# Performance work log

Measured on AMD Instinct MI355X. Metric: run time of the kernel, lower is better.

## Reference

```python
import jax, jax.numpy as jnp
import numpy as np

DIM = 1024
N_HEADS = 16
HEAD_DIM = DIM // N_HEADS  # 64
FF_DIM = 4096
BATCH = 2
SEQ = 2048
EPS = 1e-8
ROPE_BASE = 10000.0


def _rope_cos_sin(seq_len, head_dim):
    # inv_freq: [head_dim//2]
    inv_freq = 1.0 / (ROPE_BASE ** (jnp.arange(0, head_dim, 2, dtype=jnp.float32) / head_dim))
    t = jnp.arange(seq_len, dtype=jnp.float32)
    freqs = jnp.einsum('i,j->ij', t, inv_freq)          # [S, D/2]
    emb = jnp.concatenate([freqs, freqs], axis=-1)       # [S, D]
    return jnp.cos(emb), jnp.sin(emb)


def _apply_rope(x, cos, sin):
    # x: [B, S, H, D]; cos/sin: [S, D] -> broadcast [1, S, 1, D]
    d2 = x.shape[-1] // 2
    x1, x2 = x[..., :d2], x[..., d2:]
    cos = cos[None, :, None, :]
    sin = sin[None, :, None, :]
    cos1, cos2 = cos[..., :d2], cos[..., d2:]
    sin1, sin2 = sin[..., :d2], sin[..., d2:]
    return jnp.concatenate([x1 * cos1 - x2 * sin1, x1 * sin2 + x2 * cos2], axis=-1)


def _rmsnorm(x, scale):
    # norm = ||x||_2 * d^{-1/2}; out = scale * x / (norm + eps)
    norm = jnp.sqrt(jnp.sum(x * x, axis=-1, keepdims=True)) * (x.shape[-1] ** -0.5)
    return scale * x / (norm + EPS)


def setup_inputs() -> dict:
    key = jax.random.key(0)
    ks = jax.random.split(key, 10)
    s = lambda fan_in: 1.0 / np.sqrt(fan_in)
    return {
        'x': jax.random.normal(ks[0], (BATCH, SEQ, DIM), dtype=jnp.float32),
        'w_qkv': jax.random.normal(ks[1], (DIM, 3 * DIM), dtype=jnp.float32) * s(DIM),
        'w_attn_out': jax.random.normal(ks[2], (DIM, DIM), dtype=jnp.float32) * s(DIM),
        'w_gate': jax.random.normal(ks[3], (DIM, FF_DIM), dtype=jnp.float32) * s(DIM),
        'b_gate': jax.random.normal(ks[4], (FF_DIM,), dtype=jnp.float32) * 0.01,
        'w_lin': jax.random.normal(ks[5], (DIM, FF_DIM), dtype=jnp.float32) * s(DIM),
        'b_lin': jax.random.normal(ks[6], (FF_DIM,), dtype=jnp.float32) * 0.01,
        'w_ff_out': jax.random.normal(ks[7], (FF_DIM, DIM), dtype=jnp.float32) * s(FF_DIM),
        'scale1': jnp.ones((DIM,), dtype=jnp.float32),
        'scale2': jnp.ones((DIM,), dtype=jnp.float32),
    }


def reference(x, w_qkv, w_attn_out, w_gate, b_gate, w_lin, b_lin, w_ff_out, scale1, scale2):
    B, S, _ = x.shape
    residual = x
    qkv = (x @ w_qkv).reshape(B, S, 3, N_HEADS, HEAD_DIM)
    q, k, v = qkv[:, :, 0], qkv[:, :, 1], qkv[:, :, 2]  # [B, S, H, D]
    cos, sin = _rope_cos_sin(S, HEAD_DIM)
    q = _apply_rope(q, cos, sin)
    k = _apply_rope(k, cos, sin)
    # attention scores [B, H, S, S]
    attn = jnp.einsum('bqhd,bkhd->bhqk', q, k) / np.sqrt(HEAD_DIM).astype(np.float32)
    attn = jax.nn.softmax(attn, axis=-1)
    out = jnp.einsum('bhqk,bkhd->bqhd', attn, v).reshape(B, S, DIM)
    out = out @ w_attn_out
    x = _rmsnorm(residual + out, scale1)
    residual = x
    ff = jax.nn.sigmoid(x @ w_gate + b_gate) * (x @ w_lin + b_lin)
    ff = ff @ w_ff_out
    x = _rmsnorm(residual + ff, scale2)
    return x
```

## Files before the change

### kernel.cpp

```cpp
#include <hip/hip_runtime.h>
#include <stdint.h>

#define DIMN 1024
#define NH 16
#define HD 64
#define FFN 4096
#define BBATCH 2
#define SSEQ 2048
#define MROWS (BBATCH*SSEQ)

typedef __bf16 bf16;
typedef __bf16 bf16x8 __attribute__((ext_vector_type(8)));
typedef __bf16 bf16x4 __attribute__((ext_vector_type(4)));
typedef float f32x4 __attribute__((ext_vector_type(4)));
typedef float f32x16 __attribute__((ext_vector_type(16)));
typedef uint32_t u32x4 __attribute__((ext_vector_type(4)));

#define AS1 __attribute__((address_space(1)))
#define AS3 __attribute__((address_space(3)))

__device__ __forceinline__ void gload16(const bf16* g, bf16* l) {
  __builtin_amdgcn_global_load_lds((AS1 const void*)g, (AS3 void*)l, 16, 0, 0);
}

__device__ __forceinline__ uint32_t pkbf(float a, float b) {
  union { bf16 h[2]; uint32_t u; } x;
  x.h[0] = (bf16)a; x.h[1] = (bf16)b;
  return x.u;
}

__global__ void rope_table_kernel(float* __restrict__ tab) {
  int i = blockIdx.x * blockDim.x + threadIdx.x;
  int s = i >> 5, d = i & 31;
  float invf = exp2f(-(float)d * 0.4152410118609203f);
  float fr = (float)s * invf;
  tab[s*64 + d]      = cosf(fr);
  tab[s*64 + 32 + d] = sinf(fr);
}

__global__ void cast_f32_bf16(const float* __restrict__ in, bf16* __restrict__ out, int n4) {
  int i = blockIdx.x * blockDim.x + threadIdx.x;
  if (i < n4) {
    f32x4 v = ((const f32x4*)in)[i];
    bf16x4 o = {(bf16)v.x, (bf16)v.y, (bf16)v.z, (bf16)v.w};
    ((bf16x4*)out)[i] = o;
  }
}

__global__ __launch_bounds__(256) void transpose_cast_f32_bf16(
    const float* __restrict__ in, bf16* __restrict__ out, int R, int C) {
  __shared__ float t[32][33];
  int bx = blockIdx.x, by = blockIdx.y;
  int x = threadIdx.x, y = threadIdx.y;
  #pragma unroll
  for (int j = 0; j < 4; ++j) {
    int r = by*32 + y*4 + j;
    t[y*4+j][x] = in[(size_t)r*C + bx*32 + x];
  }
  __syncthreads();
  #pragma unroll
  for (int j = 0; j < 4; ++j) {
    int c = bx*32 + y*4 + j;
    out[(size_t)c*R + by*32 + x] = (bf16)t[x][y*4+j];
  }
}

template<int NP>
__global__ __launch_bounds__(256) void rmsnorm_sum_kernel(
    const float* __restrict__ parts, const float* __restrict__ resid,
    const float* __restrict__ sc,
    float* __restrict__ outf, bf16* __restrict__ outb) {
  int row = blockIdx.x;
  int tid = threadIdx.x;
  size_t off = (size_t)row * DIMN;
  f32x4 v = ((const f32x4*)(resid + off))[tid];
  #pragma unroll
  for (int p = 0; p < NP; ++p) {
    f32x4 a = ((const f32x4*)(parts + (size_t)p * MROWS * DIMN + off))[tid];
    v.x += a.x; v.y += a.y; v.z += a.z; v.w += a.w;
  }
  float ss = v.x*v.x + v.y*v.y + v.z*v.z + v.w*v.w;
  #pragma unroll
  for (int m = 1; m < 64; m <<= 1) ss += __shfl_xor(ss, m);
  __shared__ float red[4];
  if ((tid & 63) == 0) red[tid >> 6] = ss;
  __syncthreads();
  float tot = red[0] + red[1] + red[2] + red[3];
  float inv = 1.f / (sqrtf(tot) * 0.03125f + 1e-8f);
  f32x4 s4 = ((const f32x4*)sc)[tid];
  f32x4 o = {v.x*s4.x*inv, v.y*s4.y*inv, v.z*s4.z*inv, v.w*s4.w*inv};
  if (outf) ((f32x4*)(outf + off))[tid] = o;
  if (outb) {
    bf16x4 ob = {(bf16)o.x, (bf16)o.y, (bf16)o.z, (bf16)o.w};
    ((bf16x4*)(outb + off))[tid] = ob;
  }
}

template<int EPI>
__global__ void __launch_bounds__(256) gemm_bt(
    const bf16* __restrict__ A, const bf16* __restrict__ B,
    int M, int N, int K,
    void* __restrict__ o0, void* __restrict__ o1, void* __restrict__ o2,
    const void* __restrict__ a0, const void* __restrict__ a1) {
  __shared__ __align__(16) bf16 sh_a[128*32];
  __shared__ __align__(16) bf16 sh_b[128*32];
  const int tid  = threadIdx.x;
  const int lane = tid & 63;
  const int wid  = tid >> 6;

  int gx  = gridDim.x;
  int bid = blockIdx.y * gx + blockIdx.x;
  int nwg = gx * gridDim.y;
  int cpx = nwg >> 3;
  int swz = (bid & 7) * cpx + (bid >> 3);
  int bxi = swz % gx, byi = swz / gx;

  const int m0 = byi * 128, n0 = bxi * 128;
  const int wm = (wid >> 1) * 64, wn = (wid & 1) * 64;

  const int kb = blockIdx.z;
  const int KC = K / (int)gridDim.z;

  f32x4 acc[4][4] = {};

  const bf16* a_base = A + (size_t)m0 * K + (size_t)kb * KC;
  const bf16* b_base = B + (size_t)n0 * K + (size_t)kb * KC;

  for (int k0 = 0; k0 < KC; k0 += 32) {
    __syncthreads();
    #pragma unroll
    for (int i = 0; i < 2; ++i) {
      int idx = i*256 + tid;
      gload16(a_base + (size_t)(idx >> 2)*K + k0 + (idx & 3)*8, &sh_a[idx*8]);
    }
    #pragma unroll
    for (int i = 0; i < 2; ++i) {
      int idx = i*256 + tid;
      gload16(b_base + (size_t)(idx >> 2)*K + k0 + (idx & 3)*8, &sh_b[idx*8]);
    }
    __syncthreads();
    bf16x8 af[4], bfr[4];
    #pragma unroll
    for (int m = 0; m < 4; ++m)
      af[m] = *(const bf16x8*)&sh_a[(wm + m*16 + (lane & 15))*32 + (lane >> 4)*8];
    #pragma unroll
    for (int n = 0; n < 4; ++n)
      bfr[n] = *(const bf16x8*)&sh_b[(wn + n*16 + (lane & 15))*32 + (lane >> 4)*8];
    #pragma unroll
    for (int m = 0; m < 4; ++m)
      #pragma unroll
      for (int n = 0; n < 4; ++n)
        acc[m][n] = __builtin_amdgcn_mfma_f32_16x16x32_bf16(af[m], bfr[n], acc[m][n], 0, 0, 0);
  }

  const int rq = (lane >> 4) * 4;
  const int cl = lane & 15;

  if constexpr (EPI == 0) {
    bf16* q_p = (bf16*)o0; bf16* k_p = (bf16*)o1; bf16* v_p = (bf16*)o2;
    const float* rope = (const float*)a0;
    int sec = (n0 + wn) >> 10;
    int h   = ((n0 + wn) & 1023) >> 6;
    const float qsc = (sec == 0) ? 0.18033688011112042f : 1.0f;
    #pragma unroll
    for (int m = 0; m < 4; ++m) {
      #pragma unroll
      for (int reg = 0; reg < 4; ++reg) {
        int r  = m0 + wm + m*16 + rq + reg;
        int b_ = r >> 11, s_ = r & 2047;
        int tile = s_ >> 5;
        size_t tb = ((size_t)(b_*NH + h) * 64 + tile) * 2048;
        if (sec == 2) {
          int kvl = s_ & 31;
          int ks = kvl >> 4, hiv = (kvl >> 3) & 1, jv = kvl & 7;
          #pragma unroll
          for (int n = 0; n < 4; ++n) {
            int half = n >> 1;
            int qlv  = (n & 1) * 16 + cl;
            v_p[tb + (size_t)(ks*2 + half)*512 + (hiv*32 + qlv)*8 + jv] =
                (bf16)acc[m][n][reg];
          }
        } else {
          int qlt = s_ & 31;
          bf16* dst = (sec == 0 ? q_p : k_p);
          int lo = ((cl >> 3) * 32 + qlt) * 8 + (cl & 7);
          #pragma unroll
          for (int n = 0; n < 2; ++n) {
            int d1 = n*16 + cl;
            float c1 = rope[s_*64 + d1];
            float s1 = rope[s_*64 + 32 + d1];
            float x1 = acc[m][n][reg], x2 = acc[m][n+2][reg];
            dst[tb + (size_t)n*512 + lo]       = (bf16)((x1*c1 - x2*s1) * qsc);
            dst[tb + (size_t)(n+2)*512 + lo]   = (bf16)((x1*s1 + x2*c1) * qsc);
          }
        }
      }
    }
  } else if constexpr (EPI == 1) {
    float* op = (float*)o0;
    const float* rp = (const float*)a0;
    #pragma unroll
    for (int m = 0; m < 4; ++m)
      #pragma unroll
      for (int n = 0; n < 4; ++n)
        #pragma unroll
        for (int reg = 0; reg < 4; ++reg) {
          int r = m0 + wm + m*16 + rq + reg;
          int c = n0 + wn + n*16 + cl;
          op[(size_t)r*N + c] = acc[m][n][reg] + rp[(size_t)r*N + c];
        }
  } else if constexpr (EPI == 2) {
    bf16* op = (bf16*)o0;
    const float* bias = (const float*)a0;
    #pragma unroll
    for (int m = 0; m < 4; ++m)
      #pragma unroll
      for (int n = 0; n < 4; ++n)
        #pragma unroll
        for (int reg = 0; reg < 4; ++reg) {
          int r = m0 + wm + m*16 + rq + reg;
          int c = n0 + wn + n*16 + cl;
          float g = acc[m][n][reg] + bias[c];
          op[(size_t)r*N + c] = (bf16)(1.f / (1.f + __expf(-g)));
        }
  } else if constexpr (EPI == 3) {
    bf16* op = (bf16*)o0;
    const bf16* gp = (const bf16*)a0;
    const float* bias = (const float*)a1;
    #pragma unroll
    for (int m = 0; m < 4; ++m)
      #pragma unroll
      for (int n = 0; n < 4; ++n)
        #pragma unroll
        for (int reg = 0; reg < 4; ++reg) {
          int r = m0 + wm + m*16 + rq + reg;
          int c = n0 + wn + n*16 + cl;
          float l = acc[m][n][reg] + bias[c];
          op[(size_t)r*N + c] = (bf16)((float)gp[(size_t)r*N + c] * l);
        }
  } else if constexpr (EPI == 4) {
    float* op = (float*)o0 + (size_t)kb * M * N;
    #pragma unroll
    for (int m = 0; m < 4; ++m)
      #pragma unroll
      for (int n = 0; n < 4; ++n)
        #pragma unroll
        for (int reg = 0; reg < 4; ++reg) {
          int r = m0 + wm + m*16 + rq + reg;
          int c = n0 + wn + n*16 + cl;
          op[(size_t)r*N + c] = acc[m][n][reg];
        }
  }
}

__global__ void __launch_bounds__(256) attn_kernel(
    const bf16* __restrict__ qf_g, const bf16* __restrict__ kf_g,
    const bf16* __restrict__ vf_g, bf16* __restrict__ ao_g) {
  __shared__ __align__(16) bf16 lds_k[2*2048];
  __shared__ __align__(16) bf16 lds_v[2*2048];
  const int tid  = threadIdx.x;
  const int lane = tid & 63;
  const int qw   = tid >> 6;
  const int hi   = lane >> 5;
  const int ql   = lane & 31;
  const int bh   = blockIdx.y;
  const int b_   = bh >> 4, h = bh & 15;
  const int q0   = blockIdx.x * 128 + qw * 32;
  const int qt   = blockIdx.x * 4 + qw;

  const bf16* qtile = qf_g + ((size_t)bh*64 + qt) * 2048;
  const bf16* kbase = kf_g + (size_t)bh * 64 * 2048;
  const bf16* vbase = vf_g + (size_t)bh * 64 * 2048;

  bf16x8 qf[4];
  #pragma unroll
  for (int ds = 0; ds < 4; ++ds)
    qf[ds] = *(const bf16x8*)&qtile[ds*512 + lane*8];

  f32x16 o0 = {}, o1 = {};
  float lrun = 0.f;

  gload16(kbase + tid*8, &lds_k[tid*8]);
  gload16(vbase + tid*8, &lds_v[tid*8]);

  for (int t = 0; t < 64; ++t) {
    const int cur = (t & 1) * 2048;
    if (t < 63) {
      const int nxt = 2048 - cur;
      gload16(kbase + (size_t)(t+1)*2048 + tid*8, &lds_k[nxt + tid*8]);
      gload16(vbase + (size_t)(t+1)*2048 + tid*8, &lds_v[nxt + tid*8]);
      asm volatile("s_waitcnt vmcnt(2)" ::: "memory");
    } else {
      asm volatile("s_waitcnt vmcnt(0)" ::: "memory");
    }
    __builtin_amdgcn_sched_barrier(0);
    __builtin_amdgcn_s_barrier();
    __builtin_amdgcn_sched_barrier(0);

    f32x16 st = {};
    __builtin_amdgcn_s_setprio(1);
    #pragma unroll
    for (int ds = 0; ds < 4; ++ds) {
      bf16x8 kf = *(const bf16x8*)&lds_k[cur + ds*512 + lane*8];
      st = __builtin_amdgcn_mfma_f32_32x32x16_bf16(kf, qf[ds], st, 0, 0, 0);
    }
    __builtin_amdgcn_s_setprio(0);
    float p[16];
    float psum = 0.f;
    #pragma unroll
    for (int r = 0; r < 16; ++r) { p[r] = __builtin_amdgcn_exp2f(st[r]); psum += p[r]; }
    lrun += psum;

    uint32_t w0 = pkbf(p[0],p[1]),   w1 = pkbf(p[2],p[3]);
    uint32_t w2 = pkbf(p[4],p[5]),   w3 = pkbf(p[6],p[7]);
    uint32_t w4 = pkbf(p[8],p[9]),   w5 = pkbf(p[10],p[11]);
    uint32_t w6 = pkbf(p[12],p[13]), w7 = pkbf(p[14],p[15]);
    asm("v_permlane32_swap_b32 %0, %1" : "+v"(w0), "+v"(w2));
    asm("v_permlane32_swap_b32 %0, %1" : "+v"(w1), "+v"(w3));
    asm("v_permlane32_swap_b32 %0, %1" : "+v"(w4), "+v"(w6));
    asm("v_permlane32_swap_b32 %0, %1" : "+v"(w5), "+v"(w7));

    __builtin_amdgcn_s_setprio(1);
    {
      union { u32x4 u; bf16x8 b; } pu;
      u32x4 pwa = {w0, w1, w2, w3};
      pu.u = pwa;
      bf16x8 v0 = *(const bf16x8*)&lds_v[cur + 0*512 + lane*8];
      bf16x8 v1 = *(const bf16x8*)&lds_v[cur + 1*512 + lane*8];
      o0 = __builtin_amdgcn_mfma_f32_32x32x16_bf16(v0, pu.b, o0, 0, 0, 0);
      o1 = __builtin_amdgcn_mfma_f32_32x32x16_bf16(v1, pu.b, o1, 0, 0, 0);
      u32x4 pwb = {w4, w5, w6, w7};
      pu.u = pwb;
      bf16x8 v2 = *(const bf16x8*)&lds_v[cur + 2*512 + lane*8];
      bf16x8 v3 = *(const bf16x8*)&lds_v[cur + 3*512 + lane*8];
      o0 = __builtin_amdgcn_mfma_f32_32x32x16_bf16(v2, pu.b, o0, 0, 0, 0);
      o1 = __builtin_amdgcn_mfma_f32_32x32x16_bf16(v3, pu.b, o1, 0, 0, 0);
    }
    __builtin_amdgcn_s_setprio(0);

    __builtin_amdgcn_sched_barrier(0);
    __builtin_amdgcn_s_barrier();
    __builtin_amdgcn_sched_barrier(0);
  }

  lrun += __shfl_xor(lrun, 32);
  float inv = 1.f / lrun;
  bf16* aop = ao_g + ((size_t)(b_*SSEQ) + q0 + ql) * DIMN + h*HD;
  #pragma unroll
  for (int g = 0; g < 4; ++g) {
    int dbase = 8*g + 4*hi;
    bf16x4 w0 = {(bf16)(o0[4*g]*inv), (bf16)(o0[4*g+1]*inv),
                 (bf16)(o0[4*g+2]*inv), (bf16)(o0[4*g+3]*inv)};
    *(bf16x4*)&aop[dbase] = w0;
    bf16x4 w1 = {(bf16)(o1[4*g]*inv), (bf16)(o1[4*g+1]*inv),
                 (bf16)(o1[4*g+2]*inv), (bf16)(o1[4*g+3]*inv)};
    *(bf16x4*)&aop[32 + dbase] = w1;
  }
}

extern "C" void kernel_launch(void* const* d_in, const int* in_sizes, int n_in,
                              void* d_out, int out_size, void* d_ws, size_t ws_size,
                              hipStream_t stream) {
  const float* x      = (const float*)d_in[0];
  const float* w_qkv  = (const float*)d_in[1];
  const float* w_ao   = (const float*)d_in[2];
  const float* w_gate = (const float*)d_in[3];
  const float* b_gate = (const float*)d_in[4];
  const float* w_lin  = (const float*)d_in[5];
  const float* b_lin  = (const float*)d_in[6];
  const float* w_ffo  = (const float*)d_in[7];
  const float* scale1 = (const float*)d_in[8];
  const float* scale2 = (const float*)d_in[9];
  float* out = (float*)d_out;
  (void)ws_size; (void)in_sizes; (void)n_in; (void)out_size;

  uint8_t* ws = (uint8_t*)d_ws;
  bf16*  wt_ws   = (bf16*) (ws + 0);
  float* rope_ws = (float*)(ws + 8388608);
  bf16*  xb_ws   = (bf16*) (ws + 8912896);
  bf16*  ao_ws   = (bf16*) (ws + 8912896);
  bf16*  q_ws    = (bf16*) (ws + 17301504);
  bf16*  k_ws    = (bf16*) (ws + 25690112);
  bf16*  v_ws    = (bf16*) (ws + 34078720);
  float* p1_ws   = (float*)(ws + 17301504);
  bf16*  g_ws    = (bf16*) (ws + 50855936);
  bf16*  h1b_ws  = (bf16*) (ws + 84410368);
  bf16*  ffb_ws  = (bf16*) (ws + 8912896);
  float* p2_ws   = (float*)(ws + 42467328);
  float* h1f_ws  = (float*)(ws + 109576192);

  rope_table_kernel<<<256, 256, 0, stream>>>(rope_ws);
  cast_f32_bf16<<<4096, 256, 0, stream>>>(x, xb_ws, MROWS*DIMN/4);
  transpose_cast_f32_bf16<<<dim3(3*DIMN/32, DIMN/32), dim3(32,8), 0, stream>>>(w_qkv, wt_ws, DIMN, 3*DIMN);
  gemm_bt<0><<<dim3(24, 32), 256, 0, stream>>>(xb_ws, wt_ws, MROWS, 3*DIMN, DIMN,
                                               q_ws, k_ws, v_ws, rope_ws, nullptr);
  attn_kernel<<<dim3(16, 32), 256, 0, stream>>>(q_ws, k_ws, v_ws, ao_ws);
  transpose_cast_f32_bf16<<<dim3(DIMN/32, DIMN/32), dim3(32,8), 0, stream>>>(w_ao, wt_ws, DIMN, DIMN);
  gemm_bt<4><<<dim3(8, 32, 2), 256, 0, stream>>>(ao_ws, wt_ws, MROWS, DIMN, DIMN,
                                                 p1_ws, nullptr, nullptr, nullptr, nullptr);
  rmsnorm_sum_kernel<2><<<MROWS, 256, 0, stream>>>(p1_ws, x, scale1, h1f_ws, h1b_ws);
  transpose_cast_f32_bf16<<<dim3(FFN/32, DIMN/32), dim3(32,8), 0, stream>>>(w_gate, wt_ws, DIMN, FFN);
  gemm_bt<2><<<dim3(32, 32), 256, 0, stream>>>(h1b_ws, wt_ws, MROWS, FFN, DIMN,
                                               g_ws, nullptr, nullptr, b_gate, nullptr);
  transpose_cast_f32_bf16<<<dim3(FFN/32, DIMN/32), dim3(32,8), 0, stream>>>(w_lin, wt_ws, DIMN, FFN);
  gemm_bt<3><<<dim3(32, 32), 256, 0, stream>>>(h1b_ws, wt_ws, MROWS, FFN, DIMN,
                                               ffb_ws, nullptr, nullptr, g_ws, b_lin);
  transpose_cast_f32_bf16<<<dim3(DIMN/32, FFN/32), dim3(32,8), 0, stream>>>(w_ffo, wt_ws, FFN, DIMN);
  gemm_bt<4><<<dim3(8, 32, 4), 256, 0, stream>>>(ffb_ws, wt_ws, MROWS, DIMN, FFN,
                                                 p2_ws, nullptr, nullptr, nullptr, nullptr);
  rmsnorm_sum_kernel<4><<<MROWS, 256, 0, stream>>>(p2_ws, h1f_ws, scale2, out, nullptr);
}
```

Measured before the change: 366.2 us.

## Double-buffer GEMM LDS loads and fuse gate/lin GEMMs into one kernel

Every GEMM main loop now stages K-tiles into two LDS buffers and issues the next tile's async global-to-LDS loads before computing the current one, using explicit vmcnt waits and priority hints to overlap memory with MFMA. The gate and lin FFN projections are merged into one kernel that shares the A-operand fragments and keeps two accumulator sets. The epilogue applies sigmoid(gate)*lin directly, which removes the bf16 gate intermediate write and re-read and one A-matrix pass. The cost is doubled LDS and more accumulator registers in the fused kernel, which under launch_bounds(256,2) may cause spills or lower occupancy.

```diff
diff --git a/kernel.cpp b/kernel.cpp
--- a/kernel.cpp
+++ b/kernel.cpp
@@ -97,13 +97,15 @@
 }
 
 template<int EPI>
-__global__ void __launch_bounds__(256) gemm_bt(
+__global__ void __launch_bounds__(256, 2) gemm_bt(
     const bf16* __restrict__ A, const bf16* __restrict__ B,
     int M, int N, int K,
     void* __restrict__ o0, void* __restrict__ o1, void* __restrict__ o2,
     const void* __restrict__ a0, const void* __restrict__ a1) {
-  __shared__ __align__(16) bf16 sh_a[128*32];
-  __shared__ __align__(16) bf16 sh_b[128*32];
+  constexpr bool FUSED = (EPI == 5);
+  __shared__ __align__(16) bf16 sh_a[2*4096];
+  __shared__ __align__(16) bf16 sh_b[2*4096];
+  __shared__ __align__(16) bf16 sh_c[FUSED ? 2*4096 : 4];
   const int tid  = threadIdx.x;
   const int lane = tid & 63;
   const int wid  = tid >> 6;
@@ -122,35 +124,82 @@
   const int KC = K / (int)gridDim.z;
 
   f32x4 acc[4][4] = {};
+  f32x4 acc2[FUSED ? 4 : 1][FUSED ? 4 : 1] = {};
 
   const bf16* a_base = A + (size_t)m0 * K + (size_t)kb * KC;
   const bf16* b_base = B + (size_t)n0 * K + (size_t)kb * KC;
-
-  for (int k0 = 0; k0 < KC; k0 += 32) {
-    __syncthreads();
+  const bf16* c_base = nullptr;
+  if constexpr (FUSED) c_base = (const bf16*)o1 + (size_t)n0 * K;
+
+  auto stage = [&](int kt, int buf) {
+    const int lb = buf * 4096;
     #pragma unroll
     for (int i = 0; i < 2; ++i) {
       int idx = i*256 + tid;
-      gload16(a_base + (size_t)(idx >> 2)*K + k0 + (idx & 3)*8, &sh_a[idx*8]);
+      size_t go = (size_t)(idx >> 2)*K + (size_t)kt*32 + (idx & 3)*8;
+      gload16(a_base + go, &sh_a[lb + idx*8]);
     }
     #pragma unroll
     for (int i = 0; i < 2; ++i) {
       int idx = i*256 + tid;
-      gload16(b_base + (size_t)(idx >> 2)*K + k0 + (idx & 3)*8, &sh_b[idx*8]);
-    }
-    __syncthreads();
+      size_t go = (size_t)(idx >> 2)*K + (size_t)kt*32 + (idx & 3)*8;
+      gload16(b_base + go, &sh_b[lb + idx*8]);
+    }
+    if constexpr (FUSED) {
+      #pragma unroll
+      for (int i = 0; i < 2; ++i) {
+        int idx = i*256 + tid;
+        size_t go = (size_t)(idx >> 2)*K + (size_t)kt*32 + (idx & 3)*8;
+        gload16(c_base + go, &sh_c[lb + idx*8]);
+      }
+    }
+  };
+
+  const int nsteps = KC >> 5;
+  stage(0, 0);
+  for (int t = 0; t < nsteps; ++t) {
+    const int cb = t & 1;
+    if (t + 1 < nsteps) {
+      stage(t+1, cb ^ 1);
+      if constexpr (FUSED) asm volatile("s_waitcnt vmcnt(6)" ::: "memory");
+      else                 asm volatile("s_waitcnt vmcnt(4)" ::: "memory");
+    } else {
+      asm volatile("s_waitcnt vmcnt(0)" ::: "memory");
+    }
+    __builtin_amdgcn_sched_barrier(0);
+    __builtin_amdgcn_s_barrier();
+    __builtin_amdgcn_sched_barrier(0);
+
+    const int lb = cb * 4096;
     bf16x8 af[4], bfr[4];
     #pragma unroll
     for (int m = 0; m < 4; ++m)
-      af[m] = *(const bf16x8*)&sh_a[(wm + m*16 + (lane & 15))*32 + (lane >> 4)*8];
+      af[m] = *(const bf16x8*)&sh_a[lb + (wm + m*16 + (lane & 15))*32 + (lane >> 4)*8];
     #pragma unroll
     for (int n = 0; n < 4; ++n)
-      bfr[n] = *(const bf16x8*)&sh_b[(wn + n*16 + (lane & 15))*32 + (lane >> 4)*8];
+      bfr[n] = *(const bf16x8*)&sh_b[lb + (wn + n*16 + (lane & 15))*32 + (lane >> 4)*8];
+    __builtin_amdgcn_s_setprio(1);
     #pragma unroll
     for (int m = 0; m < 4; ++m)
       #pragma unroll
       for (int n = 0; n < 4; ++n)
         acc[m][n] = __builtin_amdgcn_mfma_f32_16x16x32_bf16(af[m], bfr[n], acc[m][n], 0, 0, 0);
+    __builtin_amdgcn_s_setprio(0);
+    if constexpr (FUSED) {
+      bf16x8 cf[4];
+      #pragma unroll
+      for (int n = 0; n < 4; ++n)
+        cf[n] = *(const bf16x8*)&sh_c[lb + (wn + n*16 + (lane & 15))*32 + (lane >> 4)*8];
+      __builtin_amdgcn_s_setprio(1);
+      #pragma unroll
+      for (int m = 0; m < 4; ++m)
+        #pragma unroll
+        for (int n = 0; n < 4; ++n)
+          acc2[m][n] = __builtin_amdgcn_mfma_f32_16x16x32_bf16(af[m], cf[n], acc2[m][n], 0, 0, 0);
+      __builtin_amdgcn_s_setprio(0);
+    }
+    __builtin_amdgcn_sched_barrier(0);
+    __builtin_amdgcn_s_barrier();
   }
 
   const int rq = (lane >> 4) * 4;
@@ -209,35 +258,6 @@
           int c = n0 + wn + n*16 + cl;
           op[(size_t)r*N + c] = acc[m][n][reg] + rp[(size_t)r*N + c];
         }
-  } else if constexpr (EPI == 2) {
-    bf16* op = (bf16*)o0;
-    const float* bias = (const float*)a0;
-    #pragma unroll
-    for (int m = 0; m < 4; ++m)
-      #pragma unroll
-      for (int n = 0; n < 4; ++n)
-        #pragma unroll
-        for (int reg = 0; reg < 4; ++reg) {
-          int r = m0 + wm + m*16 + rq + reg;
-          int c = n0 + wn + n*16 + cl;
-          float g = acc[m][n][reg] + bias[c];
-          op[(size_t)r*N + c] = (bf16)(1.f / (1.f + __expf(-g)));
-        }
-  } else if constexpr (EPI == 3) {
-    bf16* op = (bf16*)o0;
-    const bf16* gp = (const bf16*)a0;
-    const float* bias = (const float*)a1;
-    #pragma unroll
-    for (int m = 0; m < 4; ++m)
-      #pragma unroll
-      for (int n = 0; n < 4; ++n)
-        #pragma unroll
-        for (int reg = 0; reg < 4; ++reg) {
-          int r = m0 + wm + m*16 + rq + reg;
-          int c = n0 + wn + n*16 + cl;
-          float l = acc[m][n][reg] + bias[c];
-          op[(size_t)r*N + c] = (bf16)((float)gp[(size_t)r*N + c] * l);
-        }
   } else if constexpr (EPI == 4) {
     float* op = (float*)o0 + (size_t)kb * M * N;
     #pragma unroll
@@ -249,6 +269,23 @@
           int r = m0 + wm + m*16 + rq + reg;
           int c = n0 + wn + n*16 + cl;
           op[(size_t)r*N + c] = acc[m][n][reg];
+        }
+  } else if constexpr (EPI == 5) {
+    bf16* op = (bf16*)o0;
+    const float* bg = (const float*)a0;
+    const float* bl = (const float*)a1;
+    #pragma unroll
+    for (int m = 0; m < 4; ++m)
+      #pragma unroll
+      for (int n = 0; n < 4; ++n)
+        #pragma unroll
+        for (int reg = 0; reg < 4; ++reg) {
+          int r = m0 + wm + m*16 + rq + reg;
+          int c = n0 + wn + n*16 + cl;
+          float gv = acc[m][n][reg] + bg[c];
+          float lv = acc2[m][n][reg] + bl[c];
+          float s  = 1.f / (1.f + __expf(-gv));
+          op[(size_t)r*N + c] = (bf16)(s * lv);
         }
   }
 }
@@ -383,7 +420,7 @@
   bf16*  k_ws    = (bf16*) (ws + 25690112);
   bf16*  v_ws    = (bf16*) (ws + 34078720);
   float* p1_ws   = (float*)(ws + 17301504);
-  bf16*  g_ws    = (bf16*) (ws + 50855936);
+  bf16*  wt2_ws  = (bf16*) (ws + 50855936);
   bf16*  h1b_ws  = (bf16*) (ws + 84410368);
   bf16*  ffb_ws  = (bf16*) (ws + 8912896);
   float* p2_ws   = (float*)(ws + 42467328);
@@ -400,11 +437,9 @@
                                                  p1_ws, nullptr, nullptr, nullptr, nullptr);
   rmsnorm_sum_kernel<2><<<MROWS, 256, 0, stream>>>(p1_ws, x, scale1, h1f_ws, h1b_ws);
   transpose_cast_f32_bf16<<<dim3(FFN/32, DIMN/32), dim3(32,8), 0, stream>>>(w_gate, wt_ws, DIMN, FFN);
-  gemm_bt<2><<<dim3(32, 32), 256, 0, stream>>>(h1b_ws, wt_ws, MROWS, FFN, DIMN,
-                                               g_ws, nullptr, nullptr, b_gate, nullptr);
-  transpose_cast_f32_bf16<<<dim3(FFN/32, DIMN/32), dim3(32,8), 0, stream>>>(w_lin, wt_ws, DIMN, FFN);
-  gemm_bt<3><<<dim3(32, 32), 256, 0, stream>>>(h1b_ws, wt_ws, MROWS, FFN, DIMN,
-                                               ffb_ws, nullptr, nullptr, g_ws, b_lin);
+  transpose_cast_f32_bf16<<<dim3(FFN/32, DIMN/32), dim3(32,8), 0, stream>>>(w_lin, wt2_ws, DIMN, FFN);
+  gemm_bt<5><<<dim3(32, 32), 256, 0, stream>>>(h1b_ws, wt_ws, MROWS, FFN, DIMN,
+                                               ffb_ws, wt2_ws, nullptr, b_gate, b_lin);
   transpose_cast_f32_bf16<<<dim3(DIMN/32, FFN/32), dim3(32,8), 0, stream>>>(w_ffo, wt_ws, FFN, DIMN);
   gemm_bt<4><<<dim3(8, 32, 4), 256, 0, stream>>>(ffb_ws, wt_ws, MROWS, DIMN, FFN,
                                                  p2_ws, nullptr, nullptr, nullptr, nullptr);
```

Result: faster. 311.6 us (-14.9%).
